# Kernel tuning notes

Hardware: AMD Instinct MI355X
Metric: run time of the kernel (lower is better)

The kernel has to match this reference:

```python
import jax, jax.numpy as jnp
import numpy as np
import math

B, LQ, LK, D, DV = 16, 2048, 2048, 256, 256


def setup_inputs() -> dict:
    key = jax.random.key(0)
    k1, k2, k3, k4 = jax.random.split(key, 4)
    query = jax.random.normal(k1, (B, LQ, D), dtype=jnp.float32)
    key_t = jax.random.normal(k2, (B, LK, D), dtype=jnp.float32)
    value = jax.random.normal(k3, (B, LK, DV), dtype=jnp.float32)
    valid_length = jax.random.randint(k4, (B,), 0, LK, dtype=jnp.int32)
    return {"query": query, "key": key_t, "value": value, "valid_length": valid_length}


def reference(query, key, value, valid_length):
    # scores: [B, Lq, Lk]
    d = query.shape[-1]
    scores = jnp.einsum("bqd,bkd->bqk", query, key) / math.sqrt(d)
    # SequenceMask in the torch code sets masked positions to 0 (NOT -inf)
    # BEFORE the softmax; reproduce that exact behavior.
    kpos = jnp.arange(scores.shape[-1])  # [Lk]
    mask = kpos[None, None, :] < valid_length[:, None, None]  # [B,1,Lk] -> broadcast over Lq
    scores = jnp.where(mask, scores, 0.0)
    attn = jax.nn.softmax(scores, axis=-1)
    # Dropout is identity in eval mode.
    return jnp.einsum("bqk,bkv->bqv", attn, value)
```

## Files before the change

kernel.cpp:

```cpp
#include <hip/hip_runtime.h>

#define LQg 2048
#define LKg 2048
#define DDg 256
#define NBg 16

typedef unsigned int uint;
typedef __attribute__((ext_vector_type(8))) __bf16 bf16x8;
typedef __attribute__((ext_vector_type(16))) float f32x16;

static __device__ __forceinline__ uint pack2(float a, float b) {
    unsigned short ua = __builtin_bit_cast(unsigned short, (__bf16)a);
    unsigned short ub = __builtin_bit_cast(unsigned short, (__bf16)b);
    return (uint)ua | ((uint)ub << 16);
}

static __device__ __forceinline__ f32x16 mfma32(bf16x8 a, bf16x8 b, f32x16 c) {
    return __builtin_amdgcn_mfma_f32_32x32x16_bf16(a, b, c, 0, 0, 0);
}

static __device__ __forceinline__ int vrot(int dv) {
    return (((dv & 15) * 8) + (((dv >> 2) & 7) * 16)) & 127;
}

__global__ void tv_partial_k(const float* __restrict__ V, const int* __restrict__ vlen,
                             float* __restrict__ part) {
    const int c = blockIdx.x, b = blockIdx.y, t = threadIdx.x;
    const int vl = vlen[b];
    int bnd = ((vl + 63) >> 6) << 6;
    if (bnd > LKg) bnd = LKg;
    const int k0 = c * 128, k1 = k0 + 128;
    int lo = k0 > bnd ? k0 : bnd;
    float s = 0.f;
    for (int k = lo; k < k1; ++k) s += V[((size_t)(b * LKg + k)) * DDg + t];
    part[(size_t)(b * 16 + c) * DDg + t] = s;
}

__global__ void tv_reduce_k(const float* __restrict__ part, float* __restrict__ TV) {
    const int b = blockIdx.x, t = threadIdx.x;
    float s = 0.f;
    for (int c = 0; c < 16; ++c) s += part[(size_t)(b * 16 + c) * DDg + t];
    TV[b * DDg + t] = s;
}

__global__ __launch_bounds__(128, 1) void attn_k(
    const float* __restrict__ Qg, const float* __restrict__ Kg,
    const float* __restrict__ Vg, const int* __restrict__ vlen,
    const float* __restrict__ TV, float* __restrict__ Og, int use_tail) {
    __shared__ alignas(16) unsigned char sK[64 * 512];
    __shared__ alignas(16) unsigned char sV[256 * 128];

    const int tid = threadIdx.x;
    const int lane = tid & 63;
    const int w = tid >> 6;
    const int lq = lane & 31;
    const int h = lane >> 5;
    const int b = blockIdx.x & 15;
    const int qb = blockIdx.x >> 4;
    const int q = qb * 64 + w * 32 + lq;
    const int vl = vlen[b];

    const float SCALE = 0.09016844136f;

    bf16x8 qf[16];
    {
        const float* qp = Qg + ((size_t)(b * LQg + q)) * DDg + h * 8;
#pragma unroll
        for (int c = 0; c < 16; ++c) {
            float4 a = *(const float4*)(qp + c * 16);
            float4 bb = *(const float4*)(qp + c * 16 + 4);
            uint4 u;
            u.x = pack2(a.x * SCALE, a.y * SCALE);
            u.y = pack2(a.z * SCALE, a.w * SCALE);
            u.z = pack2(bb.x * SCALE, bb.y * SCALE);
            u.w = pack2(bb.z * SCALE, bb.w * SCALE);
            qf[c] = __builtin_bit_cast(bf16x8, u);
        }
    }

    f32x16 acc[8];
#pragma unroll
    for (int i = 0; i < 8; ++i)
#pragma unroll
        for (int j = 0; j < 16; ++j) acc[i][j] = 0.f;

    float m = -1e30f, ell = 0.f;

    const int tt = tid & 63, th = tid >> 6;
    const int swzK = (lq & 7) << 4;
    const int rotv = vrot(lq);

    const int nt = use_tail ? ((vl + 63) >> 6) : (LKg / 64);

    for (int t = 0; t < nt; ++t) {
        const int k0 = t * 64;
        __syncthreads();

        {
            const float* kp = Kg + ((size_t)(b * LKg + k0)) * DDg;
#pragma unroll
            for (int i = 0; i < 32; ++i) {
                const int row = 2 * i + th;
                const int d4 = tt * 4;
                float4 v = *(const float4*)(kp + (size_t)row * DDg + d4);
                uint2 uu;
                uu.x = pack2(v.x, v.y);
                uu.y = pack2(v.z, v.w);
                const uint off = (uint)(row * 512) + (uint)((d4 * 2) ^ ((row & 7) << 4));
                *(uint2*)(sK + off) = uu;
            }
        }
        {
            const float* vp = Vg + ((size_t)(b * LKg + k0)) * DDg;
            const int dv4 = tt * 4;
#pragma unroll
            for (int kb = 0; kb < 8; ++kb) {
                const int kbase = th * 32 + kb * 4;
                float4 r0 = *(const float4*)(vp + (size_t)(kbase + 0) * DDg + dv4);
                float4 r1 = *(const float4*)(vp + (size_t)(kbase + 1) * DDg + dv4);
                float4 r2 = *(const float4*)(vp + (size_t)(kbase + 2) * DDg + dv4);
                float4 r3 = *(const float4*)(vp + (size_t)(kbase + 3) * DDg + dv4);
                {
                    const int dv = dv4 + 0;
                    uint2 uu; uu.x = pack2(r0.x, r1.x); uu.y = pack2(r2.x, r3.x);
                    *(uint2*)(sV + (uint)(dv * 128) + (uint)((kbase * 2 + vrot(dv)) & 127)) = uu;
                }
                {
                    const int dv = dv4 + 1;
                    uint2 uu; uu.x = pack2(r0.y, r1.y); uu.y = pack2(r2.y, r3.y);
                    *(uint2*)(sV + (uint)(dv * 128) + (uint)((kbase * 2 + vrot(dv)) & 127)) = uu;
                }
                {
                    const int dv = dv4 + 2;
                    uint2 uu; uu.x = pack2(r0.z, r1.z); uu.y = pack2(r2.z, r3.z);
                    *(uint2*)(sV + (uint)(dv * 128) + (uint)((kbase * 2 + vrot(dv)) & 127)) = uu;
                }
                {
                    const int dv = dv4 + 3;
                    uint2 uu; uu.x = pack2(r0.w, r1.w); uu.y = pack2(r2.w, r3.w);
                    *(uint2*)(sV + (uint)(dv * 128) + (uint)((kbase * 2 + vrot(dv)) & 127)) = uu;
                }
            }
        }
        __syncthreads();

        f32x16 s0, s1;
#pragma unroll
        for (int j = 0; j < 16; ++j) { s0[j] = 0.f; s1[j] = 0.f; }
#pragma unroll
        for (int c = 0; c < 16; ++c) {
            const int inner = (c * 32 + h * 16) ^ swzK;
            bf16x8 kf0 = *(const bf16x8*)(sK + lq * 512 + inner);
            bf16x8 kf1 = *(const bf16x8*)(sK + (32 + lq) * 512 + inner);
            s0 = mfma32(kf0, qf[c], s0);
            s1 = mfma32(kf1, qf[c], s1);
        }

        const bool full = (k0 + 64 <= vl);
        if (!full) {
            const int kb0 = k0 + 4 * h;
#pragma unroll
            for (int r = 0; r < 16; ++r) {
                const int key0 = kb0 + (r & 3) + 8 * (r >> 2);
                if (key0 >= vl) s0[r] = 0.f;
                if (key0 + 32 >= vl) s1[r] = 0.f;
            }
        }

        float mt = s0[0];
#pragma unroll
        for (int r = 1; r < 16; ++r) mt = fmaxf(mt, s0[r]);
#pragma unroll
        for (int r = 0; r < 16; ++r) mt = fmaxf(mt, s1[r]);
        mt = fmaxf(mt, __shfl_xor(mt, 32));
        if (mt > m + 8.f) {
            const float mn = fmaxf(m, mt);
            const float sf = exp2f(m - mn);
            ell *= sf;
#pragma unroll
            for (int i = 0; i < 8; ++i) acc[i] *= sf;
            m = mn;
        }
        float rs = 0.f;
#pragma unroll
        for (int r = 0; r < 16; ++r) { s0[r] = exp2f(s0[r] - m); rs += s0[r]; }
#pragma unroll
        for (int r = 0; r < 16; ++r) { s1[r] = exp2f(s1[r] - m); rs += s1[r]; }
        rs += __shfl_xor(rs, 32);
        ell += rs;

        bf16x8 pf[4];
#pragma unroll
        for (int kc = 0; kc < 4; ++kc) {
            const f32x16& ps = (kc < 2) ? s0 : s1;
            const int bb = (kc & 1) * 8;
            uint w0 = pack2(ps[bb + 0], ps[bb + 1]);
            uint w1 = pack2(ps[bb + 2], ps[bb + 3]);
            uint w2 = pack2(ps[bb + 4], ps[bb + 5]);
            uint w3 = pack2(ps[bb + 6], ps[bb + 7]);
            uint t0 = __shfl_xor(w0, 32);
            uint t1 = __shfl_xor(w1, 32);
            uint t2 = __shfl_xor(w2, 32);
            uint t3 = __shfl_xor(w3, 32);
            uint4 u;
            u.x = h ? t2 : w0;
            u.y = h ? t3 : w1;
            u.z = h ? w2 : t0;
            u.w = h ? w3 : t1;
            pf[kc] = __builtin_bit_cast(bf16x8, u);
        }

#pragma unroll
        for (int kc = 0; kc < 4; ++kc) {
            const int kk = kc * 16 + h * 8;
            const int o0 = (kk * 2 + rotv) & 127;
            const int o1 = ((kk + 4) * 2 + rotv) & 127;
#pragma unroll
            for (int dt = 0; dt < 8; ++dt) {
                const uint base = (uint)(dt * 4096 + lq * 128);
                uint2 a = *(const uint2*)(sV + base + (uint)o0);
                uint2 c2 = *(const uint2*)(sV + base + (uint)o1);
                uint4 u; u.x = a.x; u.y = a.y; u.z = c2.x; u.w = c2.y;
                acc[dt] = mfma32(__builtin_bit_cast(bf16x8, u), pf[kc], acc[dt]);
            }
        }
    }

    if (use_tail) {
        const int bnd = nt * 64;
        const int cnt = LKg - bnd;
        if (cnt > 0) {
            if (m < -8.f) {
                const float sf = exp2f(m);
                ell *= sf;
#pragma unroll
                for (int i = 0; i < 8; ++i) acc[i] *= sf;
                m = 0.f;
            }
            const float pt = exp2f(-m);
            ell += (float)cnt * pt;
            const float* tp = TV + b * DDg + h * 4;
#pragma unroll
            for (int dt = 0; dt < 8; ++dt) {
#pragma unroll
                for (int rg = 0; rg < 4; ++rg) {
                    float4 tv = *(const float4*)(tp + dt * 32 + rg * 8);
                    acc[dt][rg * 4 + 0] += pt * tv.x;
                    acc[dt][rg * 4 + 1] += pt * tv.y;
                    acc[dt][rg * 4 + 2] += pt * tv.z;
                    acc[dt][rg * 4 + 3] += pt * tv.w;
                }
            }
        }
    }

    const float inv = 1.f / ell;
    float* op = Og + ((size_t)(b * LQg + q)) * DDg + h * 4;
#pragma unroll
    for (int dt = 0; dt < 8; ++dt) {
#pragma unroll
        for (int rg = 0; rg < 4; ++rg) {
            float4 o;
            o.x = acc[dt][rg * 4 + 0] * inv;
            o.y = acc[dt][rg * 4 + 1] * inv;
            o.z = acc[dt][rg * 4 + 2] * inv;
            o.w = acc[dt][rg * 4 + 3] * inv;
            *(float4*)(op + dt * 32 + rg * 8) = o;
        }
    }
}

extern "C" void kernel_launch(void* const* d_in, const int* in_sizes, int n_in,
                              void* d_out, int out_size, void* d_ws, size_t ws_size,
                              hipStream_t stream) {
    const float* Q = (const float*)d_in[0];
    const float* K = (const float*)d_in[1];
    const float* V = (const float*)d_in[2];
    const int* vlen = (const int*)d_in[3];
    float* out = (float*)d_out;

    float* part = (float*)d_ws;
    float* TV = (float*)((char*)d_ws + (size_t)NBg * 16 * DDg * sizeof(float));
    const size_t need = (size_t)NBg * 16 * DDg * 4 + (size_t)NBg * DDg * 4;
    const int use_tail = (ws_size >= need) ? 1 : 0;

    if (use_tail) {
        tv_partial_k<<<dim3(16, 16), 256, 0, stream>>>(V, vlen, part);
        tv_reduce_k<<<dim3(16), 256, 0, stream>>>(part, TV);
    }
    attn_k<<<dim3(512), dim3(128), 0, stream>>>(Q, K, V, vlen, TV, out, use_tail);
}
```

Measured before the change: 192.6 us.

## Split KV range across blocks with flash-decoding style combine kernel

Blocks now grow to 256 threads covering 128 queries, and the key range is split into up to four chunks across a second grid dimension. Each split writes bf16 partial accumulators plus running max and sum to workspace, and a new combine kernel merges them with the masked-tail contribution. The aim is to balance work across CUs when valid lengths vary by batch, and to share K/V staging across more waves. In exchange it adds workspace traffic for bf16 partials, an extra kernel launch, and a rounding step on the partial accumulators. The split only runs when the workspace is large enough.

Measured after the change: 430.8 us. 2.24x slower.

```diff
diff --git a/kernel.cpp b/kernel.cpp
--- a/kernel.cpp
+++ b/kernel.cpp
@@ -4,14 +4,16 @@
 #define LKg 2048
 #define DDg 256
 #define NBg 16
+#define SMAX 4
 
 typedef unsigned int uint;
+typedef unsigned short ushort;
 typedef __attribute__((ext_vector_type(8))) __bf16 bf16x8;
 typedef __attribute__((ext_vector_type(16))) float f32x16;
 
 static __device__ __forceinline__ uint pack2(float a, float b) {
-    unsigned short ua = __builtin_bit_cast(unsigned short, (__bf16)a);
-    unsigned short ub = __builtin_bit_cast(unsigned short, (__bf16)b);
+    ushort ua = __builtin_bit_cast(ushort, (__bf16)a);
+    ushort ub = __builtin_bit_cast(ushort, (__bf16)b);
     return (uint)ua | ((uint)ub << 16);
 }
 
@@ -43,10 +45,12 @@
     TV[b * DDg + t] = s;
 }
 
-__global__ __launch_bounds__(128, 1) void attn_k(
+__global__ __launch_bounds__(256, 2) void attn_k(
     const float* __restrict__ Qg, const float* __restrict__ Kg,
     const float* __restrict__ Vg, const int* __restrict__ vlen,
-    const float* __restrict__ TV, float* __restrict__ Og, int use_tail) {
+    const float* __restrict__ TV, float* __restrict__ Og,
+    ushort* __restrict__ Pacc, float* __restrict__ Mp, float* __restrict__ Ep,
+    int S, int use_tail) {
     __shared__ alignas(16) unsigned char sK[64 * 512];
     __shared__ alignas(16) unsigned char sV[256 * 128];
 
@@ -57,10 +61,25 @@
     const int h = lane >> 5;
     const int b = blockIdx.x & 15;
     const int qb = blockIdx.x >> 4;
-    const int q = qb * 64 + w * 32 + lq;
+    const int s = blockIdx.y;
+    const int q = qb * 128 + w * 32 + lq;
     const int vl = vlen[b];
 
     const float SCALE = 0.09016844136f;
+
+    const int nt = use_tail ? ((vl + 63) >> 6) : (LKg / 64);
+    const int chunk = (nt + S - 1) / S;
+    const int t0 = s * chunk;
+    const int t1 = (t0 + chunk < nt) ? (t0 + chunk) : nt;
+
+    if (S > 1 && t0 >= t1) {
+        if (h == 0) {
+            const size_t pidx = ((size_t)(s * NBg + b)) * LQg + q;
+            Mp[pidx] = -1e30f;
+            Ep[pidx] = 0.f;
+        }
+        return;
+    }
 
     bf16x8 qf[16];
     {
@@ -90,17 +109,15 @@
     const int swzK = (lq & 7) << 4;
     const int rotv = vrot(lq);
 
-    const int nt = use_tail ? ((vl + 63) >> 6) : (LKg / 64);
-
-    for (int t = 0; t < nt; ++t) {
+    for (int t = t0; t < t1; ++t) {
         const int k0 = t * 64;
         __syncthreads();
 
         {
             const float* kp = Kg + ((size_t)(b * LKg + k0)) * DDg;
 #pragma unroll
-            for (int i = 0; i < 32; ++i) {
-                const int row = 2 * i + th;
+            for (int i = 0; i < 16; ++i) {
+                const int row = 4 * i + th;
                 const int d4 = tt * 4;
                 float4 v = *(const float4*)(kp + (size_t)row * DDg + d4);
                 uint2 uu;
@@ -114,8 +131,8 @@
             const float* vp = Vg + ((size_t)(b * LKg + k0)) * DDg;
             const int dv4 = tt * 4;
 #pragma unroll
-            for (int kb = 0; kb < 8; ++kb) {
-                const int kbase = th * 32 + kb * 4;
+            for (int kb = 0; kb < 4; ++kb) {
+                const int kbase = th * 16 + kb * 4;
                 float4 r0 = *(const float4*)(vp + (size_t)(kbase + 0) * DDg + dv4);
                 float4 r1 = *(const float4*)(vp + (size_t)(kbase + 1) * DDg + dv4);
                 float4 r2 = *(const float4*)(vp + (size_t)(kbase + 2) * DDg + dv4);
@@ -198,15 +215,15 @@
             uint w1 = pack2(ps[bb + 2], ps[bb + 3]);
             uint w2 = pack2(ps[bb + 4], ps[bb + 5]);
             uint w3 = pack2(ps[bb + 6], ps[bb + 7]);
-            uint t0 = __shfl_xor(w0, 32);
-            uint t1 = __shfl_xor(w1, 32);
-            uint t2 = __shfl_xor(w2, 32);
-            uint t3 = __shfl_xor(w3, 32);
+            uint e0 = __shfl_xor(w0, 32);
+            uint e1 = __shfl_xor(w1, 32);
+            uint e2 = __shfl_xor(w2, 32);
+            uint e3 = __shfl_xor(w3, 32);
             uint4 u;
-            u.x = h ? t2 : w0;
-            u.y = h ? t3 : w1;
-            u.z = h ? w2 : t0;
-            u.w = h ? w3 : t1;
+            u.x = h ? e2 : w0;
+            u.y = h ? e3 : w1;
+            u.z = h ? w2 : e0;
+            u.w = h ? w3 : e1;
             pf[kc] = __builtin_bit_cast(bf16x8, u);
         }
 
@@ -224,6 +241,24 @@
                 acc[dt] = mfma32(__builtin_bit_cast(bf16x8, u), pf[kc], acc[dt]);
             }
         }
+    }
+
+    if (S > 1) {
+        const size_t pidx = ((size_t)(s * NBg + b)) * LQg + q;
+        if (h == 0) { Mp[pidx] = m; Ep[pidx] = ell; }
+        ushort* pp = Pacc + pidx * DDg;
+#pragma unroll
+        for (int dt = 0; dt < 8; ++dt) {
+#pragma unroll
+            for (int rg = 0; rg < 4; ++rg) {
+                const int dv0 = dt * 32 + 8 * rg + 4 * h;
+                uint2 uu;
+                uu.x = pack2(acc[dt][rg * 4 + 0], acc[dt][rg * 4 + 1]);
+                uu.y = pack2(acc[dt][rg * 4 + 2], acc[dt][rg * 4 + 3]);
+                *(uint2*)(pp + dv0) = uu;
+            }
+        }
+        return;
     }
 
     if (use_tail) {
@@ -253,7 +288,6 @@
             }
         }
     }
-
     const float inv = 1.f / ell;
     float* op = Og + ((size_t)(b * LQg + q)) * DDg + h * 4;
 #pragma unroll
@@ -268,6 +302,53 @@
             *(float4*)(op + dt * 32 + rg * 8) = o;
         }
     }
+}
+
+__global__ void combine_k(const ushort* __restrict__ Pacc, const float* __restrict__ Mp,
+                          const float* __restrict__ Ep, const float* __restrict__ TV,
+                          const int* __restrict__ vlen, float* __restrict__ Og, int S) {
+    const int t = threadIdx.x;
+    const int qi = t >> 6;
+    const int dv4 = (t & 63) * 4;
+    const long long bq0 = (long long)blockIdx.x * 4;
+    const int b = (int)(bq0 >> 11);
+    const int q = (int)(bq0 & 2047) + qi;
+    const int vl = vlen[b];
+    int bnd = ((vl + 63) >> 6) << 6;
+    if (bnd > LKg) bnd = LKg;
+    const int cnt = LKg - bnd;
+
+    float mi[SMAX], ei[SMAX];
+    float M = (cnt > 0) ? 0.f : -1e30f;
+    for (int s = 0; s < S; ++s) {
+        const size_t pidx = ((size_t)(s * NBg + b)) * LQg + q;
+        mi[s] = Mp[pidx];
+        ei[s] = Ep[pidx];
+        if (ei[s] > 0.f) M = fmaxf(M, mi[s]);
+    }
+    float L = 0.f;
+    float o0 = 0.f, o1 = 0.f, o2 = 0.f, o3 = 0.f;
+    for (int s = 0; s < S; ++s) {
+        if (ei[s] > 0.f) {
+            const float wg = exp2f(mi[s] - M);
+            L += ei[s] * wg;
+            const size_t pidx = ((size_t)(s * NBg + b)) * LQg + q;
+            uint2 uu = *(const uint2*)(Pacc + pidx * DDg + dv4);
+            o0 += wg * __builtin_bit_cast(float, (uu.x & 0xFFFFu) << 16);
+            o1 += wg * __builtin_bit_cast(float, (uu.x & 0xFFFF0000u));
+            o2 += wg * __builtin_bit_cast(float, (uu.y & 0xFFFFu) << 16);
+            o3 += wg * __builtin_bit_cast(float, (uu.y & 0xFFFF0000u));
+        }
+    }
+    if (cnt > 0) {
+        const float pt = exp2f(-M);
+        L += (float)cnt * pt;
+        float4 tv = *(const float4*)(TV + b * DDg + dv4);
+        o0 += pt * tv.x; o1 += pt * tv.y; o2 += pt * tv.z; o3 += pt * tv.w;
+    }
+    const float inv = 1.f / L;
+    float4 o; o.x = o0 * inv; o.y = o1 * inv; o.z = o2 * inv; o.w = o3 * inv;
+    *(float4*)(Og + ((size_t)(b * LQg + q)) * DDg + dv4) = o;
 }
 
 extern "C" void kernel_launch(void* const* d_in, const int* in_sizes, int n_in,
@@ -279,14 +360,31 @@
     const int* vlen = (const int*)d_in[3];
     float* out = (float*)d_out;
 
-    float* part = (float*)d_ws;
-    float* TV = (float*)((char*)d_ws + (size_t)NBg * 16 * DDg * sizeof(float));
-    const size_t need = (size_t)NBg * 16 * DDg * 4 + (size_t)NBg * DDg * 4;
-    const int use_tail = (ws_size >= need) ? 1 : 0;
+    const size_t off_part = 0;
+    const size_t off_TV = off_part + (size_t)NBg * 16 * DDg * 4;
+    const size_t off_M = off_TV + (size_t)NBg * DDg * 4;
+    const size_t off_E = off_M + (size_t)SMAX * NBg * LQg * 4;
+    const size_t off_acc = off_E + (size_t)SMAX * NBg * LQg * 4;
+    const size_t acc_per_split = (size_t)NBg * LQg * DDg * 2;
+
+    int S = 1, use_tail = 0;
+    if (ws_size >= off_acc + 4 * acc_per_split) { S = 4; use_tail = 1; }
+    else if (ws_size >= off_acc + 2 * acc_per_split) { S = 2; use_tail = 1; }
+    else if (ws_size >= off_M) { S = 1; use_tail = 1; }
+
+    float* part = (float*)((char*)d_ws + off_part);
+    float* TV = (float*)((char*)d_ws + off_TV);
+    float* Mp = (float*)((char*)d_ws + off_M);
+    float* Ep = (float*)((char*)d_ws + off_E);
+    ushort* Pacc = (ushort*)((char*)d_ws + off_acc);
 
     if (use_tail) {
         tv_partial_k<<<dim3(16, 16), 256, 0, stream>>>(V, vlen, part);
         tv_reduce_k<<<dim3(16), 256, 0, stream>>>(part, TV);
     }
-    attn_k<<<dim3(512), dim3(128), 0, stream>>>(Q, K, V, vlen, TV, out, use_tail);
-}
+    attn_k<<<dim3(256, S), dim3(256), 0, stream>>>(Q, K, V, vlen, TV, out,
+                                                   Pacc, Mp, Ep, S, use_tail);
+    if (S > 1) {
+        combine_k<<<dim3(NBg * LQg / 4), dim3(256), 0, stream>>>(Pacc, Mp, Ep, TV, vlen, out, S);
+    }
+}
```

## Pre-convert K/V to bf16 swizzled tiles and double-buffer via direct global-to-LDS loads

Applied to the files above, without the earlier changes.

Adds prep kernels that convert K and V once into bf16 tile images already laid out in the LDS swizzle, then streams those tiles into double-buffered shared memory with global_load_lds while computing the previous tile. The KV tile shrinks from 64 to 32 keys, there is one barrier per iteration, and the block-to-batch mapping changes so consecutive blocks share a batch. This removes per-block redundant fp32 conversion and transposition of K/V and overlaps loads with MFMA work. In exchange it adds two extra launches and workspace traffic, and prep converts all keys, including masked ones.

New measurement: 203.6 us. +5.7%, slower.

```diff
diff --git a/kernel.cpp b/kernel.cpp
--- a/kernel.cpp
+++ b/kernel.cpp
@@ -4,14 +4,18 @@
 #define LKg 2048
 #define DDg 256
 #define NBg 16
+#define KVB 32
+#define NTILES 64
 
 typedef unsigned int uint;
+typedef unsigned short ushort;
+typedef unsigned char uchar;
 typedef __attribute__((ext_vector_type(8))) __bf16 bf16x8;
 typedef __attribute__((ext_vector_type(16))) float f32x16;
 
 static __device__ __forceinline__ uint pack2(float a, float b) {
-    unsigned short ua = __builtin_bit_cast(unsigned short, (__bf16)a);
-    unsigned short ub = __builtin_bit_cast(unsigned short, (__bf16)b);
+    ushort ua = __builtin_bit_cast(ushort, (__bf16)a);
+    ushort ub = __builtin_bit_cast(ushort, (__bf16)b);
     return (uint)ua | ((uint)ub << 16);
 }
 
@@ -19,15 +23,56 @@
     return __builtin_amdgcn_mfma_f32_32x32x16_bf16(a, b, c, 0, 0, 0);
 }
 
-static __device__ __forceinline__ int vrot(int dv) {
-    return (((dv & 15) * 8) + (((dv >> 2) & 7) * 16)) & 127;
+typedef const __attribute__((address_space(1))) uchar* gas_t;
+typedef __attribute__((address_space(3))) uchar* las_t;
+static __device__ __forceinline__ void gl_lds16(const void* g, void* l) {
+    __builtin_amdgcn_global_load_lds((gas_t)g, (las_t)l, 16, 0, 0);
+}
+
+__global__ __launch_bounds__(256) void prep_k(const float* __restrict__ K,
+                                              uchar* __restrict__ Kimg) {
+    const uint gid = blockIdx.x * 256 + threadIdx.x;
+    const uint d8 = gid & 31;
+    const uint row = (gid >> 5) & 31;
+    const uint t = (gid >> 10) & 63;
+    const uint b = gid >> 16;
+    const float* src = K + (((size_t)b * LKg + t * KVB + row) * DDg + d8 * 8);
+    float4 a = *(const float4*)src;
+    float4 c = *(const float4*)(src + 4);
+    uint4 u;
+    u.x = pack2(a.x, a.y); u.y = pack2(a.z, a.w);
+    u.z = pack2(c.x, c.y); u.w = pack2(c.z, c.w);
+    const size_t base = ((size_t)(b * NTILES + t)) << 14;
+    const uint off = row * 512 + ((d8 * 16) ^ ((row & 7) << 4));
+    *(uint4*)(Kimg + base + off) = u;
+}
+
+__global__ __launch_bounds__(256) void prep_v(const float* __restrict__ V,
+                                              uchar* __restrict__ Vimg) {
+    const uint gid = blockIdx.x * 256 + threadIdx.x;
+    const uint dv = gid & 255;
+    const uint t = (gid >> 8) & 63;
+    const uint b = gid >> 14;
+    const uint rot = 4 * ((dv >> 1) & 15);
+    uchar* base = Vimg + (((size_t)(b * NTILES + t)) << 14) + dv * 64;
+    const float* src = V + ((size_t)b * LKg + t * KVB) * DDg + dv;
+#pragma unroll
+    for (int kq = 0; kq < 8; ++kq) {
+        float v0 = src[(kq * 4 + 0) * DDg];
+        float v1 = src[(kq * 4 + 1) * DDg];
+        float v2 = src[(kq * 4 + 2) * DDg];
+        float v3 = src[(kq * 4 + 3) * DDg];
+        const uint o = (8 * kq + rot) & 63;
+        *(uint*)(base + o) = pack2(v0, v1);
+        *(uint*)(base + ((o + 4) & 63)) = pack2(v2, v3);
+    }
 }
 
 __global__ void tv_partial_k(const float* __restrict__ V, const int* __restrict__ vlen,
                              float* __restrict__ part) {
     const int c = blockIdx.x, b = blockIdx.y, t = threadIdx.x;
     const int vl = vlen[b];
-    int bnd = ((vl + 63) >> 6) << 6;
+    int bnd = ((vl + 31) >> 5) << 5;
     if (bnd > LKg) bnd = LKg;
     const int k0 = c * 128, k1 = k0 + 128;
     int lo = k0 > bnd ? k0 : bnd;
@@ -43,24 +88,43 @@
     TV[b * DDg + t] = s;
 }
 
+template <int IMG>
 __global__ __launch_bounds__(128, 1) void attn_k(
     const float* __restrict__ Qg, const float* __restrict__ Kg,
-    const float* __restrict__ Vg, const int* __restrict__ vlen,
+    const float* __restrict__ Vg, const uchar* __restrict__ Kimg,
+    const uchar* __restrict__ Vimg, const int* __restrict__ vlen,
     const float* __restrict__ TV, float* __restrict__ Og, int use_tail) {
-    __shared__ alignas(16) unsigned char sK[64 * 512];
-    __shared__ alignas(16) unsigned char sV[256 * 128];
+    __shared__ alignas(16) uchar sK[2][KVB * 512];
+    __shared__ alignas(16) uchar sV[2][256 * 64];
 
     const int tid = threadIdx.x;
     const int lane = tid & 63;
     const int w = tid >> 6;
     const int lq = lane & 31;
     const int h = lane >> 5;
-    const int b = blockIdx.x & 15;
-    const int qb = blockIdx.x >> 4;
+    const int b = blockIdx.x >> 5;
+    const int qb = blockIdx.x & 31;
     const int q = qb * 64 + w * 32 + lq;
     const int vl = vlen[b];
 
     const float SCALE = 0.09016844136f;
+
+    const int nt = use_tail ? ((vl + KVB - 1) / KVB) : NTILES;
+    const int swzK = (lq & 7) << 4;
+    const int rotv = (lq >> 1) * 4;
+
+    int cur = 0;
+    if (nt > 0) {
+        if (IMG) {
+            const uchar* gK = Kimg + (((size_t)(b * NTILES + 0)) << 14) + tid * 16;
+            const uchar* gV = Vimg + (((size_t)(b * NTILES + 0)) << 14) + tid * 16;
+#pragma unroll
+            for (int i = 0; i < 8; ++i) {
+                gl_lds16(gK + i * 2048, &sK[0][i * 2048 + tid * 16]);
+                gl_lds16(gV + i * 2048, &sV[0][i * 2048 + tid * 16]);
+            }
+        }
+    }
 
     bf16x8 qf[16];
     {
@@ -78,6 +142,38 @@
         }
     }
 
+    if (!IMG && nt > 0) {
+#pragma unroll
+        for (int i = 0; i < 8; ++i) {
+            const int cid = i * 128 + tid;
+            const int d8 = cid & 31, row = cid >> 5;
+            const float* src = Kg + (((size_t)b * LKg + row) * DDg + d8 * 8);
+            float4 a = *(const float4*)src;
+            float4 c = *(const float4*)(src + 4);
+            uint4 u;
+            u.x = pack2(a.x, a.y); u.y = pack2(a.z, a.w);
+            u.z = pack2(c.x, c.y); u.w = pack2(c.z, c.w);
+            *(uint4*)(&sK[0][row * 512 + ((d8 * 16) ^ ((row & 7) << 4))]) = u;
+        }
+#pragma unroll
+        for (int i = 0; i < 2; ++i) {
+            const int dv = i * 128 + tid;
+            const uint rot = 4 * ((dv >> 1) & 15);
+            const float* src = Vg + (size_t)b * LKg * DDg + dv;
+            uchar* dst = &sV[0][dv * 64];
+#pragma unroll
+            for (int kq = 0; kq < 8; ++kq) {
+                float v0 = src[(kq * 4 + 0) * DDg];
+                float v1 = src[(kq * 4 + 1) * DDg];
+                float v2 = src[(kq * 4 + 2) * DDg];
+                float v3 = src[(kq * 4 + 3) * DDg];
+                const uint o = (8 * kq + rot) & 63;
+                *(uint*)(dst + o) = pack2(v0, v1);
+                *(uint*)(dst + ((o + 4) & 63)) = pack2(v2, v3);
+            }
+        }
+    }
+
     f32x16 acc[8];
 #pragma unroll
     for (int i = 0; i < 8; ++i)
@@ -86,92 +182,77 @@
 
     float m = -1e30f, ell = 0.f;
 
-    const int tt = tid & 63, th = tid >> 6;
-    const int swzK = (lq & 7) << 4;
-    const int rotv = vrot(lq);
-
-    const int nt = use_tail ? ((vl + 63) >> 6) : (LKg / 64);
+    __syncthreads();
 
     for (int t = 0; t < nt; ++t) {
-        const int k0 = t * 64;
-        __syncthreads();
-
-        {
-            const float* kp = Kg + ((size_t)(b * LKg + k0)) * DDg;
-#pragma unroll
-            for (int i = 0; i < 32; ++i) {
-                const int row = 2 * i + th;
-                const int d4 = tt * 4;
-                float4 v = *(const float4*)(kp + (size_t)row * DDg + d4);
-                uint2 uu;
-                uu.x = pack2(v.x, v.y);
-                uu.y = pack2(v.z, v.w);
-                const uint off = (uint)(row * 512) + (uint)((d4 * 2) ^ ((row & 7) << 4));
-                *(uint2*)(sK + off) = uu;
-            }
-        }
-        {
-            const float* vp = Vg + ((size_t)(b * LKg + k0)) * DDg;
-            const int dv4 = tt * 4;
-#pragma unroll
-            for (int kb = 0; kb < 8; ++kb) {
-                const int kbase = th * 32 + kb * 4;
-                float4 r0 = *(const float4*)(vp + (size_t)(kbase + 0) * DDg + dv4);
-                float4 r1 = *(const float4*)(vp + (size_t)(kbase + 1) * DDg + dv4);
-                float4 r2 = *(const float4*)(vp + (size_t)(kbase + 2) * DDg + dv4);
-                float4 r3 = *(const float4*)(vp + (size_t)(kbase + 3) * DDg + dv4);
-                {
-                    const int dv = dv4 + 0;
-                    uint2 uu; uu.x = pack2(r0.x, r1.x); uu.y = pack2(r2.x, r3.x);
-                    *(uint2*)(sV + (uint)(dv * 128) + (uint)((kbase * 2 + vrot(dv)) & 127)) = uu;
+        const int k0 = t * KVB;
+
+        if (t + 1 < nt) {
+            if (IMG) {
+                const uchar* gK = Kimg + (((size_t)(b * NTILES + t + 1)) << 14) + tid * 16;
+                const uchar* gV = Vimg + (((size_t)(b * NTILES + t + 1)) << 14) + tid * 16;
+#pragma unroll
+                for (int i = 0; i < 8; ++i) {
+                    gl_lds16(gK + i * 2048, &sK[cur ^ 1][i * 2048 + tid * 16]);
+                    gl_lds16(gV + i * 2048, &sV[cur ^ 1][i * 2048 + tid * 16]);
                 }
-                {
-                    const int dv = dv4 + 1;
-                    uint2 uu; uu.x = pack2(r0.y, r1.y); uu.y = pack2(r2.y, r3.y);
-                    *(uint2*)(sV + (uint)(dv * 128) + (uint)((kbase * 2 + vrot(dv)) & 127)) = uu;
+            } else {
+                const int k1 = (t + 1) * KVB;
+#pragma unroll
+                for (int i = 0; i < 8; ++i) {
+                    const int cid = i * 128 + tid;
+                    const int d8 = cid & 31, row = cid >> 5;
+                    const float* src = Kg + (((size_t)b * LKg + k1 + row) * DDg + d8 * 8);
+                    float4 a = *(const float4*)src;
+                    float4 c = *(const float4*)(src + 4);
+                    uint4 u;
+                    u.x = pack2(a.x, a.y); u.y = pack2(a.z, a.w);
+                    u.z = pack2(c.x, c.y); u.w = pack2(c.z, c.w);
+                    *(uint4*)(&sK[cur ^ 1][row * 512 + ((d8 * 16) ^ ((row & 7) << 4))]) = u;
                 }
-                {
-                    const int dv = dv4 + 2;
-                    uint2 uu; uu.x = pack2(r0.z, r1.z); uu.y = pack2(r2.z, r3.z);
-                    *(uint2*)(sV + (uint)(dv * 128) + (uint)((kbase * 2 + vrot(dv)) & 127)) = uu;
+#pragma unroll
+                for (int i = 0; i < 2; ++i) {
+                    const int dv = i * 128 + tid;
+                    const uint rot = 4 * ((dv >> 1) & 15);
+                    const float* src = Vg + ((size_t)b * LKg + k1) * DDg + dv;
+                    uchar* dst = &sV[cur ^ 1][dv * 64];
+#pragma unroll
+                    for (int kq = 0; kq < 8; ++kq) {
+                        float v0 = src[(kq * 4 + 0) * DDg];
+                        float v1 = src[(kq * 4 + 1) * DDg];
+                        float v2 = src[(kq * 4 + 2) * DDg];
+                        float v3 = src[(kq * 4 + 3) * DDg];
+                        const uint o = (8 * kq + rot) & 63;
+                        *(uint*)(dst + o) = pack2(v0, v1);
+                        *(uint*)(dst + ((o + 4) & 63)) = pack2(v2, v3);
+                    }
                 }
-                {
-                    const int dv = dv4 + 3;
-                    uint2 uu; uu.x = pack2(r0.w, r1.w); uu.y = pack2(r2.w, r3.w);
-                    *(uint2*)(sV + (uint)(dv * 128) + (uint)((kbase * 2 + vrot(dv)) & 127)) = uu;
-                }
-            }
-        }
-        __syncthreads();
-
-        f32x16 s0, s1;
-#pragma unroll
-        for (int j = 0; j < 16; ++j) { s0[j] = 0.f; s1[j] = 0.f; }
+            }
+        }
+
+        const uchar* sKc = sK[cur];
+        const uchar* sVc = sV[cur];
+        f32x16 s0;
+#pragma unroll
+        for (int j = 0; j < 16; ++j) s0[j] = 0.f;
 #pragma unroll
         for (int c = 0; c < 16; ++c) {
-            const int inner = (c * 32 + h * 16) ^ swzK;
-            bf16x8 kf0 = *(const bf16x8*)(sK + lq * 512 + inner);
-            bf16x8 kf1 = *(const bf16x8*)(sK + (32 + lq) * 512 + inner);
-            s0 = mfma32(kf0, qf[c], s0);
-            s1 = mfma32(kf1, qf[c], s1);
-        }
-
-        const bool full = (k0 + 64 <= vl);
-        if (!full) {
+            bf16x8 kf = *(const bf16x8*)(sKc + lq * 512 + ((c * 32 + h * 16) ^ swzK));
+            s0 = mfma32(kf, qf[c], s0);
+        }
+
+        if (k0 + KVB > vl) {
             const int kb0 = k0 + 4 * h;
 #pragma unroll
             for (int r = 0; r < 16; ++r) {
                 const int key0 = kb0 + (r & 3) + 8 * (r >> 2);
                 if (key0 >= vl) s0[r] = 0.f;
-                if (key0 + 32 >= vl) s1[r] = 0.f;
             }
         }
 
         float mt = s0[0];
 #pragma unroll
         for (int r = 1; r < 16; ++r) mt = fmaxf(mt, s0[r]);
-#pragma unroll
-        for (int r = 0; r < 16; ++r) mt = fmaxf(mt, s1[r]);
         mt = fmaxf(mt, __shfl_xor(mt, 32));
         if (mt > m + 8.f) {
             const float mn = fmaxf(m, mt);
@@ -184,50 +265,54 @@
         float rs = 0.f;
 #pragma unroll
         for (int r = 0; r < 16; ++r) { s0[r] = exp2f(s0[r] - m); rs += s0[r]; }
-#pragma unroll
-        for (int r = 0; r < 16; ++r) { s1[r] = exp2f(s1[r] - m); rs += s1[r]; }
         rs += __shfl_xor(rs, 32);
         ell += rs;
 
-        bf16x8 pf[4];
-#pragma unroll
-        for (int kc = 0; kc < 4; ++kc) {
-            const f32x16& ps = (kc < 2) ? s0 : s1;
-            const int bb = (kc & 1) * 8;
-            uint w0 = pack2(ps[bb + 0], ps[bb + 1]);
-            uint w1 = pack2(ps[bb + 2], ps[bb + 3]);
-            uint w2 = pack2(ps[bb + 4], ps[bb + 5]);
-            uint w3 = pack2(ps[bb + 6], ps[bb + 7]);
-            uint t0 = __shfl_xor(w0, 32);
-            uint t1 = __shfl_xor(w1, 32);
-            uint t2 = __shfl_xor(w2, 32);
-            uint t3 = __shfl_xor(w3, 32);
+        bf16x8 pf[2];
+#pragma unroll
+        for (int kc = 0; kc < 2; ++kc) {
+            const int bb = kc * 8;
+            uint w0 = pack2(s0[bb + 0], s0[bb + 1]);
+            uint w1 = pack2(s0[bb + 2], s0[bb + 3]);
+            uint w2 = pack2(s0[bb + 4], s0[bb + 5]);
+            uint w3 = pack2(s0[bb + 6], s0[bb + 7]);
+            uint e0 = __shfl_xor(w0, 32);
+            uint e1 = __shfl_xor(w1, 32);
+            uint e2 = __shfl_xor(w2, 32);
+            uint e3 = __shfl_xor(w3, 32);
             uint4 u;
-            u.x = h ? t2 : w0;
-            u.y = h ? t3 : w1;
-            u.z = h ? w2 : t0;
-            u.w = h ? w3 : t1;
+            u.x = h ? e2 : w0;
+            u.y = h ? e3 : w1;
+            u.z = h ? w2 : e0;
+            u.w = h ? w3 : e1;
             pf[kc] = __builtin_bit_cast(bf16x8, u);
         }
 
 #pragma unroll
-        for (int kc = 0; kc < 4; ++kc) {
+        for (int kc = 0; kc < 2; ++kc) {
             const int kk = kc * 16 + h * 8;
-            const int o0 = (kk * 2 + rotv) & 127;
-            const int o1 = ((kk + 4) * 2 + rotv) & 127;
+            const uint o0 = (uint)((2 * kk + rotv) & 63);
+            const uint o1 = (uint)((2 * kk + 4 + rotv) & 63);
+            const uint o2 = (uint)((2 * kk + 8 + rotv) & 63);
+            const uint o3 = (uint)((2 * kk + 12 + rotv) & 63);
 #pragma unroll
             for (int dt = 0; dt < 8; ++dt) {
-                const uint base = (uint)(dt * 4096 + lq * 128);
-                uint2 a = *(const uint2*)(sV + base + (uint)o0);
-                uint2 c2 = *(const uint2*)(sV + base + (uint)o1);
-                uint4 u; u.x = a.x; u.y = a.y; u.z = c2.x; u.w = c2.y;
+                const uchar* base = sVc + dt * 2048 + lq * 64;
+                uint4 u;
+                u.x = *(const uint*)(base + o0);
+                u.y = *(const uint*)(base + o1);
+                u.z = *(const uint*)(base + o2);
+                u.w = *(const uint*)(base + o3);
                 acc[dt] = mfma32(__builtin_bit_cast(bf16x8, u), pf[kc], acc[dt]);
             }
         }
+
+        __syncthreads();
+        cur ^= 1;
     }
 
     if (use_tail) {
-        const int bnd = nt * 64;
+        const int bnd = nt * KVB;
         const int cnt = LKg - bnd;
         if (cnt > 0) {
             if (m < -8.f) {
@@ -279,14 +364,31 @@
     const int* vlen = (const int*)d_in[3];
     float* out = (float*)d_out;
 
-    float* part = (float*)d_ws;
-    float* TV = (float*)((char*)d_ws + (size_t)NBg * 16 * DDg * sizeof(float));
-    const size_t need = (size_t)NBg * 16 * DDg * 4 + (size_t)NBg * DDg * 4;
-    const int use_tail = (ws_size >= need) ? 1 : 0;
+    const size_t off_part = 0;
+    const size_t off_TV = 262144;
+    const size_t off_K = 524288;
+    const size_t imgsz = (size_t)NBg * NTILES * 16384;
+    const size_t off_V = off_K + imgsz;
+    const size_t need_tail = off_TV + (size_t)NBg * DDg * 4;
+    const size_t need_img = off_V + imgsz;
+
+    const int use_tail = (ws_size >= need_tail) ? 1 : 0;
+    const int use_img = (ws_size >= need_img) ? 1 : 0;
+
+    float* part = (float*)((char*)d_ws + off_part);
+    float* TV = (float*)((char*)d_ws + off_TV);
+    uchar* Kimg = (uchar*)d_ws + off_K;
+    uchar* Vimg = (uchar*)d_ws + off_V;
 
     if (use_tail) {
         tv_partial_k<<<dim3(16, 16), 256, 0, stream>>>(V, vlen, part);
         tv_reduce_k<<<dim3(16), 256, 0, stream>>>(part, TV);
     }
-    attn_k<<<dim3(512), dim3(128), 0, stream>>>(Q, K, V, vlen, TV, out, use_tail);
-}
+    if (use_img) {
+        prep_k<<<dim3(4096), 256, 0, stream>>>(K, Kimg);
+        prep_v<<<dim3(1024), 256, 0, stream>>>(V, Vimg);
+        attn_k<1><<<dim3(512), 128, 0, stream>>>(Q, K, V, Kimg, Vimg, vlen, TV, out, use_tail);
+    } else {
+        attn_k<0><<<dim3(512), 128, 0, stream>>>(Q, K, V, Kimg, Vimg, vlen, TV, out, use_tail);
+    }
+}
```
